# Optimization experiments

Hardware: AMD Instinct MI355X
Metric: run time of the kernel (lower is better)

The kernel has to match this reference:

```python
import jax, jax.numpy as jnp
import numpy as np

# ---- static ragged-batch / paging layout (known at trace time) ----
B = 4
Q_LENS = np.array([256, 512, 128, 384])        # new tokens per sequence
HIST = np.array([1792, 1024, 1536, 768])       # cached history per sequence
KV_LENS = Q_LENS + HIST
BS = 64                                        # paged-cache block size
NUM_BLOCKS = 128
H, D = 32, 128
HID = H * D
TOTAL_Q = int(Q_LENS.sum())                    # 1280 packed tokens
MAX_Q = int(Q_LENS.max())
MAX_KV = int(KV_LENS.max())
NBLK = (KV_LENS + BS - 1) // BS
MAX_BLOCKS = int(NBLK.max())                   # 32
ROPE_BASE = 10000.0

Q_START = np.concatenate([[0], np.cumsum(Q_LENS)[:-1]])
TOK_SEQ = np.repeat(np.arange(B), Q_LENS)                      # [TOTAL_Q]
TOK_LOCAL = np.concatenate([np.arange(l) for l in Q_LENS])     # [TOTAL_Q]
TOK_POS = (HIST[TOK_SEQ] + TOK_LOCAL).astype(np.int32)         # absolute positions

_perm = np.random.RandomState(0).permutation(NUM_BLOCKS)
BLOCK_TABLE = np.zeros((B, MAX_BLOCKS), np.int32)
_o = 0
for _i in range(B):
    BLOCK_TABLE[_i, :NBLK[_i]] = _perm[_o:_o + NBLK[_i]]
    _o += NBLK[_i]

_j = np.arange(MAX_Q)
# position of each padded query row; 0 for pad rows so the softmax row stays finite
POS_PAD = np.where(_j[None, :] < Q_LENS[:, None], HIST[:, None] + _j[None, :], 0)
KV_IDX = np.arange(MAX_KV)


def rope(x, pos):
    """HF-Llama rotary embedding on [T, heads, D] at absolute positions pos [T]."""
    half = D // 2
    inv_freq = 1.0 / (ROPE_BASE ** (jnp.arange(0, D, 2, dtype=jnp.float32) / D))
    ang = pos[:, None].astype(jnp.float32) * inv_freq[None, :]          # [T, D/2]
    cos = jnp.concatenate([jnp.cos(ang), jnp.cos(ang)], -1)[:, None, :]  # [T,1,D]
    sin = jnp.concatenate([jnp.sin(ang), jnp.sin(ang)], -1)[:, None, :]
    x1, x2 = x[..., :half], x[..., half:]
    rot = jnp.concatenate([-x2, x1], -1)                                 # rotate_half
    return x * cos + rot * sin


def setup_inputs() -> dict:
    key = jax.random.key(0)
    ks = jax.random.split(key, 7)
    s = 1.0 / np.sqrt(HID)
    return {
        'hidden_states': jax.random.normal(ks[0], (TOTAL_Q, HID), jnp.float32),
        'wq': jax.random.normal(ks[1], (HID, HID), jnp.float32) * s,
        'wk': jax.random.normal(ks[2], (HID, HID), jnp.float32) * s,
        'wv': jax.random.normal(ks[3], (HID, HID), jnp.float32) * s,
        'wo': jax.random.normal(ks[4], (HID, HID), jnp.float32) * s,
        'past_key': jax.random.normal(ks[5], (NUM_BLOCKS, BS, H, D), jnp.float32),
        'past_value': jax.random.normal(ks[6], (NUM_BLOCKS, BS, H, D), jnp.float32),
        'position_ids': jnp.asarray(TOK_POS, jnp.int32),
        'block_offsets': jnp.asarray(BLOCK_TABLE, jnp.int32),
    }


def reference(hidden_states, wq, wk, wv, wo, past_key, past_value,
              position_ids, block_offsets):
    # qkv projections (Linear without bias: x @ W.T)
    q = (hidden_states @ wq.T).reshape(TOTAL_Q, H, D)
    k = (hidden_states @ wk.T).reshape(TOTAL_Q, H, D)
    v = (hidden_states @ wv.T).reshape(TOTAL_Q, H, D)
    # inline RoPE at absolute (history + local) positions
    q = rope(q, position_ids)
    k = rope(k, position_ids)
    # fill paged KV cache via block table (context.fill_cache)
    dest = block_offsets[TOK_SEQ, position_ids // BS] * BS + position_ids % BS
    kc = past_key.reshape(NUM_BLOCKS * BS, H, D).at[dest].set(k)
    vc = past_value.reshape(NUM_BLOCKS * BS, H, D).at[dest].set(v)
    # paged gather of ragged KV per sequence: [B, MAX_KV, H, D]
    gath = block_offsets[:, KV_IDX // BS] * BS + KV_IDX[None, :] % BS
    K = kc[gath]
    V = vc[gath]
    # pad packed queries to [B, MAX_Q, H, D]
    Qp = jnp.zeros((B, MAX_Q, H, D), q.dtype).at[TOK_SEQ, TOK_LOCAL].set(q)
    scores = jnp.einsum('bqhd,bkhd->bhqk', Qp, K) / jnp.sqrt(jnp.float32(D))
    mask = KV_IDX[None, None, :] <= POS_PAD[:, :, None]   # causal + per-seq kv_len
    scores = jnp.where(mask[:, None, :, :], scores, jnp.float32(-1e30))
    attn = jax.nn.softmax(scores, axis=-1)
    out = jnp.einsum('bhqk,bkhd->bqhd', attn, V)
    # back to packed layout and output projection
    out = out[TOK_SEQ, TOK_LOCAL].reshape(TOTAL_Q, HID)
    return out @ wo.T
```

## Files before the change

### kernel.cpp

```cpp
#include <hip/hip_runtime.h>
#include <stdint.h>


typedef __attribute__((ext_vector_type(8))) short bf16x8;
typedef __attribute__((ext_vector_type(4))) float f32x4;
typedef __attribute__((ext_vector_type(4))) unsigned int u32x4;

__device__ __forceinline__ unsigned short f2bf(float f) {
  unsigned int u = __float_as_uint(f);
  u += 0x7fffu + ((u >> 16) & 1u);
  return (unsigned short)(u >> 16);
}

__global__ __launch_bounds__(256) void cvt_bf16(const float* __restrict__ src,
                                                unsigned short* __restrict__ dst, int n4) {
  int i = blockIdx.x * 256 + threadIdx.x;
  if (i >= n4) return;
  float4 v = ((const float4*)src)[i];
  ushort4 o;
  o.x = f2bf(v.x); o.y = f2bf(v.y); o.z = f2bf(v.z); o.w = f2bf(v.w);
  ((ushort4*)dst)[i] = o;
}

__device__ __forceinline__ void gload16(const void* g, void* l) {
  __builtin_amdgcn_global_load_lds(
      (const __attribute__((address_space(1))) unsigned int*)(g),
      (__attribute__((address_space(3))) unsigned int*)(l), 16, 0, 0);
}

__global__ __launch_bounds__(512, 2) void gemm256(const unsigned short* __restrict__ A,
                                                  const unsigned short* __restrict__ B,
                                                  float* __restrict__ C, int N, int K) {
  extern __shared__ char lds[];
  const int tid = threadIdx.x;
  const int lane = tid & 63;
  const int wid = tid >> 6;
  const int wm = wid >> 2, wn = wid & 3;
  const int qcol = lane & 15, g = lane >> 4;
  const int mbase = blockIdx.y * 256, nbase = blockIdx.x * 256;
  const long Kb = (long)K * 2;

  const int srow = tid >> 3;
  const int scb = ((tid & 7) * 16) ^ (((srow >> 2) & 3) << 5);
  const char* Ab = (const char*)A;
  const char* Bb = (const char*)B;
  const long asrc0 = (long)(mbase + srow) * Kb + scb;
  const long asrc1 = (long)(mbase + 64 + srow) * Kb + scb;
  const long asrc2 = (long)(mbase + 128 + srow) * Kb + scb;
  const long asrc3 = (long)(mbase + 192 + srow) * Kb + scb;
  const long bsrc0 = (long)(nbase + srow) * Kb + scb;
  const long bsrc1 = (long)(nbase + 64 + srow) * Kb + scb;
  const long bsrc2 = (long)(nbase + 128 + srow) * Kb + scb;
  const long bsrc3 = (long)(nbase + 192 + srow) * Kb + scb;
  const int dst0 = tid * 16;

#define STAGE256(kt, bs) {                                                   \
    long ko = (long)(kt) * 128;                                              \
    char* Lw = lds + (bs) * 32768;                                           \
    gload16(Ab + asrc0 + ko, Lw + dst0);                                     \
    gload16(Ab + asrc1 + ko, Lw + 8192 + dst0);                              \
    gload16(Ab + asrc2 + ko, Lw + 16384 + dst0);                             \
    gload16(Ab + asrc3 + ko, Lw + 24576 + dst0);                             \
    gload16(Bb + bsrc0 + ko, Lw + 65536 + dst0);                             \
    gload16(Bb + bsrc1 + ko, Lw + 65536 + 8192 + dst0);                      \
    gload16(Bb + bsrc2 + ko, Lw + 65536 + 16384 + dst0);                     \
    gload16(Bb + bsrc3 + ko, Lw + 65536 + 24576 + dst0);                     \
  }

  const int swl = ((qcol >> 2) & 3) << 5;
  const int c0 = (g * 16) ^ swl;
  const int c1 = (64 + g * 16) ^ swl;
  const int aoff = (wm * 128 + qcol) * 128;
  const int boff = 65536 + (wn * 64 + qcol) * 128;

  f32x4 acc[8][4];
#pragma unroll
  for (int i = 0; i < 8; ++i)
#pragma unroll
    for (int j = 0; j < 4; ++j) { acc[i][j][0]=0.f; acc[i][j][1]=0.f; acc[i][j][2]=0.f; acc[i][j][3]=0.f; }

  STAGE256(0, 0);
  const int nkt = K >> 6;
#pragma unroll 1
  for (int kt = 0; kt < nkt; ++kt) {
    const int cur = kt & 1;
    const char* Lc = lds + cur * 32768;
    if (kt + 1 < nkt) {
      STAGE256(kt + 1, cur ^ 1);
      asm volatile("s_waitcnt vmcnt(8)" ::: "memory");
    } else {
      asm volatile("s_waitcnt vmcnt(0)" ::: "memory");
    }
    __builtin_amdgcn_sched_barrier(0);
    __builtin_amdgcn_s_barrier();
    __builtin_amdgcn_sched_barrier(0);

    bf16x8 af[4][2], bfr[4][2];
#pragma unroll
    for (int mi = 0; mi < 4; ++mi) {
      af[mi][0] = *(const bf16x8*)(Lc + aoff + mi * 2048 + c0);
      af[mi][1] = *(const bf16x8*)(Lc + aoff + mi * 2048 + c1);
    }
#pragma unroll
    for (int ni = 0; ni < 2; ++ni) {
      bfr[ni][0] = *(const bf16x8*)(Lc + boff + ni * 2048 + c0);
      bfr[ni][1] = *(const bf16x8*)(Lc + boff + ni * 2048 + c1);
    }
    asm volatile("s_waitcnt lgkmcnt(0)" ::: "memory");
    __builtin_amdgcn_sched_barrier(0);
    __builtin_amdgcn_s_setprio(1);
#pragma unroll
    for (int mi = 0; mi < 4; ++mi)
#pragma unroll
      for (int ni = 0; ni < 2; ++ni) {
        acc[mi][ni] = __builtin_amdgcn_mfma_f32_16x16x32_bf16(af[mi][0], bfr[ni][0], acc[mi][ni], 0, 0, 0);
        acc[mi][ni] = __builtin_amdgcn_mfma_f32_16x16x32_bf16(af[mi][1], bfr[ni][1], acc[mi][ni], 0, 0, 0);
      }
    __builtin_amdgcn_s_setprio(0);
#pragma unroll
    for (int ni = 2; ni < 4; ++ni) {
      bfr[ni][0] = *(const bf16x8*)(Lc + boff + ni * 2048 + c0);
      bfr[ni][1] = *(const bf16x8*)(Lc + boff + ni * 2048 + c1);
    }
    asm volatile("s_waitcnt lgkmcnt(0)" ::: "memory");
    __builtin_amdgcn_sched_barrier(0);
    __builtin_amdgcn_s_setprio(1);
#pragma unroll
    for (int mi = 0; mi < 4; ++mi)
#pragma unroll
      for (int ni = 2; ni < 4; ++ni) {
        acc[mi][ni] = __builtin_amdgcn_mfma_f32_16x16x32_bf16(af[mi][0], bfr[ni][0], acc[mi][ni], 0, 0, 0);
        acc[mi][ni] = __builtin_amdgcn_mfma_f32_16x16x32_bf16(af[mi][1], bfr[ni][1], acc[mi][ni], 0, 0, 0);
      }
    __builtin_amdgcn_s_setprio(0);
#pragma unroll
    for (int mi = 0; mi < 4; ++mi) {
      af[mi][0] = *(const bf16x8*)(Lc + aoff + (mi + 4) * 2048 + c0);
      af[mi][1] = *(const bf16x8*)(Lc + aoff + (mi + 4) * 2048 + c1);
    }
    asm volatile("s_waitcnt lgkmcnt(0)" ::: "memory");
    __builtin_amdgcn_sched_barrier(0);
    __builtin_amdgcn_s_setprio(1);
#pragma unroll
    for (int mi = 0; mi < 4; ++mi)
#pragma unroll
      for (int ni = 2; ni < 4; ++ni) {
        acc[mi + 4][ni] = __builtin_amdgcn_mfma_f32_16x16x32_bf16(af[mi][0], bfr[ni][0], acc[mi + 4][ni], 0, 0, 0);
        acc[mi + 4][ni] = __builtin_amdgcn_mfma_f32_16x16x32_bf16(af[mi][1], bfr[ni][1], acc[mi + 4][ni], 0, 0, 0);
      }
    __builtin_amdgcn_s_setprio(0);
    __builtin_amdgcn_s_setprio(1);
#pragma unroll
    for (int mi = 0; mi < 4; ++mi)
#pragma unroll
      for (int ni = 0; ni < 2; ++ni) {
        acc[mi + 4][ni] = __builtin_amdgcn_mfma_f32_16x16x32_bf16(af[mi][0], bfr[ni][0], acc[mi + 4][ni], 0, 0, 0);
        acc[mi + 4][ni] = __builtin_amdgcn_mfma_f32_16x16x32_bf16(af[mi][1], bfr[ni][1], acc[mi + 4][ni], 0, 0, 0);
      }
    __builtin_amdgcn_s_setprio(0);
    __builtin_amdgcn_s_barrier();
    __builtin_amdgcn_sched_barrier(0);
  }
#undef STAGE256
  const int crow = mbase + wm * 128 + g * 4;
  const int ccol = nbase + wn * 64 + qcol;
#pragma unroll
  for (int mi = 0; mi < 8; ++mi)
#pragma unroll
    for (int ni = 0; ni < 4; ++ni)
#pragma unroll
      for (int r = 0; r < 4; ++r)
        C[(long)(crow + mi * 16 + r) * N + (ccol + ni * 16)] = acc[mi][ni][r];
}

__global__ __launch_bounds__(256, 2) void gemm_bt(const unsigned short* __restrict__ A,
                                                  const unsigned short* __restrict__ B,
                                                  float* __restrict__ C, int N, int K) {
  __shared__ unsigned short As[128 * 32] __attribute__((aligned(16)));
  __shared__ unsigned short Bs[128 * 32] __attribute__((aligned(16)));
  const int tid = threadIdx.x;
  const int lane = tid & 63;
  const int wv = tid >> 6;
  const int wr = wv >> 1, wc = wv & 1;
  const int mbase = blockIdx.y * 128, nbase = blockIdx.x * 128;
  const int r16 = lane >> 2;
  const int k8 = (lane & 3) * 8;
  const unsigned short* Ag0 = A + (mbase + wv * 32 + r16) * K + k8;
  const unsigned short* Ag1 = Ag0 + 16 * K;
  const unsigned short* Bg0 = B + (nbase + wv * 32 + r16) * K + k8;
  const unsigned short* Bg1 = Bg0 + 16 * K;
  unsigned short* Asl = As + wv * 1024 + lane * 8;
  unsigned short* Bsl = Bs + wv * 1024 + lane * 8;
  f32x4 acc[4][4];
#pragma unroll
  for (int i = 0; i < 4; ++i)
#pragma unroll
    for (int j = 0; j < 4; ++j) { acc[i][j][0]=0.f; acc[i][j][1]=0.f; acc[i][j][2]=0.f; acc[i][j][3]=0.f; }
  const int rowA = (wr * 64 + (lane & 15)) * 32 + (lane >> 4) * 8;
  const int colB = (wc * 64 + (lane & 15)) * 32 + (lane >> 4) * 8;
  for (int kt = 0; kt < K; kt += 32) {
    gload16(Ag0 + kt, Asl);
    gload16(Ag1 + kt, Asl + 512);
    gload16(Bg0 + kt, Bsl);
    gload16(Bg1 + kt, Bsl + 512);
    __syncthreads();
    bf16x8 af[4], bfr[4];
#pragma unroll
    for (int mi = 0; mi < 4; ++mi) af[mi] = *(const bf16x8*)(As + rowA + mi * 512);
#pragma unroll
    for (int ni = 0; ni < 4; ++ni) bfr[ni] = *(const bf16x8*)(Bs + colB + ni * 512);
#pragma unroll
    for (int mi = 0; mi < 4; ++mi)
#pragma unroll
      for (int ni = 0; ni < 4; ++ni)
        acc[mi][ni] = __builtin_amdgcn_mfma_f32_16x16x32_bf16(af[mi], bfr[ni], acc[mi][ni], 0, 0, 0);
    __syncthreads();
  }
  const int crow = mbase + wr * 64 + (lane >> 4) * 4;
  const int ccol = nbase + wc * 64 + (lane & 15);
#pragma unroll
  for (int mi = 0; mi < 4; ++mi)
#pragma unroll
    for (int ni = 0; ni < 4; ++ni)
#pragma unroll
      for (int r = 0; r < 4; ++r)
        C[(long)(crow + mi * 16 + r) * N + (ccol + ni * 16)] = acc[mi][ni][r];
}

__global__ __launch_bounds__(256) void rope_qk(const float* __restrict__ qkv, const int* __restrict__ pos,
                                               unsigned short* __restrict__ Qb, unsigned short* __restrict__ Kg) {
  int gw = blockIdx.x * 4 + (threadIdx.x >> 6);
  int lane = threadIdx.x & 63;
  int t = gw >> 5, h = gw & 31;
  int p = pos[t];
  int b = (t < 256) ? 0 : (t < 768) ? 1 : (t < 896) ? 2 : 3;
  float invf = exp2f(-(float)lane * 0.2076205059304601f);
  float ang = (float)p * invf;
  float sv = sinf(ang), cv = cosf(ang);
  const float* src = qkv + (long)t * 12288 + h * 128 + lane;
  float q1 = src[0], q2 = src[64];
  float k1 = src[4096], k2 = src[4096 + 64];
  const float scl = 0.08838834764831845f;
  unsigned short* qd = Qb + (long)t * 4096 + h * 128 + lane;
  qd[0]  = f2bf((q1 * cv - q2 * sv) * scl);
  qd[64] = f2bf((q2 * cv + q1 * sv) * scl);
  unsigned short* kd = Kg + ((long)(b * 32 + h) * 2048 + p) * 128 + lane;
  kd[0]  = f2bf(k1 * cv - k2 * sv);
  kd[64] = f2bf(k2 * cv + k1 * sv);
}

__global__ __launch_bounds__(256) void v_scatter(const float* __restrict__ qkv, unsigned short* __restrict__ VgT) {
  int tt = blockIdx.x, h = blockIdx.y;
  int b = (tt < 4) ? 0 : (tt < 12) ? 1 : (tt < 14) ? 2 : 3;
  int q0 = (b == 0) ? 0 : (b == 1) ? 256 : (b == 2) ? 768 : 896;
  int hist = (b == 0) ? 1792 : (b == 1) ? 1024 : (b == 2) ? 1536 : 768;
  int t0 = tt * 64;
  int jb = hist + t0 - q0;
  __shared__ unsigned short vt[64][130];
  int tid = threadIdx.x;
  int jj0 = tid >> 5, c4 = (tid & 31) * 4;
#pragma unroll
  for (int ps = 0; ps < 8; ++ps) {
    int jj = jj0 + ps * 8;
    float4 v = *(const float4*)(qkv + (long)(t0 + jj) * 12288 + 8192 + h * 128 + c4);
    ushort2 a, c;
    a.x = f2bf(v.x); a.y = f2bf(v.y); c.x = f2bf(v.z); c.y = f2bf(v.w);
    *(ushort2*)&vt[jj][c4] = a;
    *(ushort2*)&vt[jj][c4 + 2] = c;
  }
  __syncthreads();
  int d = tid >> 1, half = tid & 1;
  unsigned short* dst = VgT + ((long)(b * 32 + h) * 128 + d) * 2048 + jb + half * 32;
  int j0 = half * 32;
#pragma unroll
  for (int w = 0; w < 4; ++w) {
    uint4 u;
    u.x = vt[j0 + w * 8 + 0][d] | ((unsigned)vt[j0 + w * 8 + 1][d] << 16);
    u.y = vt[j0 + w * 8 + 2][d] | ((unsigned)vt[j0 + w * 8 + 3][d] << 16);
    u.z = vt[j0 + w * 8 + 4][d] | ((unsigned)vt[j0 + w * 8 + 5][d] << 16);
    u.w = vt[j0 + w * 8 + 6][d] | ((unsigned)vt[j0 + w * 8 + 7][d] << 16);
    ((uint4*)dst)[w] = u;
  }
}

__global__ __launch_bounds__(256) void gather_hist(const float* __restrict__ pk, const float* __restrict__ pv,
                                                   const int* __restrict__ btab,
                                                   unsigned short* __restrict__ Kg, unsigned short* __restrict__ VgT) {
  int gx = blockIdx.x, h = blockIdx.y;
  int b = (gx < 28) ? 0 : (gx < 44) ? 1 : (gx < 68) ? 2 : 3;
  int jt = gx - ((b == 0) ? 0 : (b == 1) ? 28 : (b == 2) ? 44 : 68);
  int slot0 = btab[b * 32 + jt] * 64;
  int jbase = jt * 64;
  __shared__ unsigned short vt[64][130];
  int tid = threadIdx.x;
  int jj0 = tid >> 5, c4 = (tid & 31) * 4;
#pragma unroll
  for (int ps = 0; ps < 8; ++ps) {
    int jj = jj0 + ps * 8;
    long off = ((long)(slot0 + jj) * 32 + h) * 128 + c4;
    float4 kk = *(const float4*)(pk + off);
    ushort4 ko;
    ko.x = f2bf(kk.x); ko.y = f2bf(kk.y); ko.z = f2bf(kk.z); ko.w = f2bf(kk.w);
    *(ushort4*)(Kg + ((long)(b * 32 + h) * 2048 + jbase + jj) * 128 + c4) = ko;
    float4 vv = *(const float4*)(pv + off);
    ushort2 a, c;
    a.x = f2bf(vv.x); a.y = f2bf(vv.y); c.x = f2bf(vv.z); c.y = f2bf(vv.w);
    *(ushort2*)&vt[jj][c4] = a;
    *(ushort2*)&vt[jj][c4 + 2] = c;
  }
  __syncthreads();
  int d = tid >> 1, half = tid & 1;
  unsigned short* dst = VgT + ((long)(b * 32 + h) * 128 + d) * 2048 + jbase + half * 32;
  int j0 = half * 32;
#pragma unroll
  for (int w = 0; w < 4; ++w) {
    uint4 u;
    u.x = vt[j0 + w * 8 + 0][d] | ((unsigned)vt[j0 + w * 8 + 1][d] << 16);
    u.y = vt[j0 + w * 8 + 2][d] | ((unsigned)vt[j0 + w * 8 + 3][d] << 16);
    u.z = vt[j0 + w * 8 + 4][d] | ((unsigned)vt[j0 + w * 8 + 5][d] << 16);
    u.w = vt[j0 + w * 8 + 6][d] | ((unsigned)vt[j0 + w * 8 + 7][d] << 16);
    ((uint4*)dst)[w] = u;
  }
}

__global__ __launch_bounds__(256) void attn_part(const unsigned short* __restrict__ Qb,
                                                 const unsigned short* __restrict__ Kg,
                                                 const unsigned short* __restrict__ VgT,
                                                 const int* __restrict__ pos,
                                                 float* __restrict__ Opart,
                                                 float* __restrict__ ml) {
  __shared__ char lds[32768] __attribute__((aligned(16)));
  int qt = blockIdx.x, h = blockIdx.y, ck = blockIdx.z;
  int tid = threadIdx.x;
  int wv = tid >> 6, lane = tid & 63;
  int b = (qt < 4) ? 0 : (qt < 12) ? 1 : (qt < 14) ? 2 : 3;
  int qb = qt * 64 + wv * 16;
  int qcol = lane & 15, g = lane >> 4;
  int t = qb + qcol;
  int p = pos[t];
  int pmax_wave = pos[qb + 15];
  int pmax_blk = pos[qt * 64 + 63];
  int kv_begin = ck * 512;
  if (kv_begin > pmax_blk) return;
  int kv_end = pmax_blk + 1;
  if (kv_end > kv_begin + 512) kv_end = kv_begin + 512;
  int nt = (kv_end - kv_begin + 31) >> 5;

  const char* KbhB = (const char*)(Kg + (long)(b * 32 + h) * 2048 * 128);
  const char* VbhB = (const char*)(VgT + (long)(b * 32 + h) * 128 * 2048);

  const int d0 = tid * 16, d1 = 4096 + tid * 16;
  const int ksrc0 = d0 ^ (((d0 >> 8) & 7) << 4);
  const int ksrc1 = d1 ^ (((d1 >> 8) & 7) << 4);
  const int vrow0 = d0 >> 6, vrow1 = d1 >> 6;
  const int vsrc0 = vrow0 * 4096 + ((d0 & 63) ^ ((vrow0 & 3) << 4));
  const int vsrc1 = vrow1 * 4096 + ((d1 & 63) ^ ((vrow1 & 3) << 4));

#define STAGE(kv0, buf)                                                     \
  {                                                                          \
    const char* Ksrc = KbhB + (long)(kv0) * 256;                             \
    const char* Vsrc = VbhB + (long)(kv0) * 2;                               \
    char* Kd = lds + (buf) * 8192;                                           \
    char* Vd = lds + 16384 + (buf) * 8192;                                   \
    gload16(Ksrc + ksrc0, Kd + d0);                                          \
    gload16(Ksrc + ksrc1, Kd + d1);                                          \
    gload16(Vsrc + vsrc0, Vd + d0);                                          \
    gload16(Vsrc + vsrc1, Vd + d1);                                          \
  }

  const unsigned short* Qp = Qb + (long)t * 4096 + h * 128 + g * 8;
  bf16x8 qf[4];
#pragma unroll
  for (int c = 0; c < 4; ++c) qf[c] = *(const bf16x8*)(Qp + c * 32);

  const int kswz = ((qcol & 7) << 4);
  const int vswz = (g * 16) ^ ((qcol & 3) << 4);

  float m = -1e30f, lsum = 0.f;
  f32x4 o[8];
#pragma unroll
  for (int i = 0; i < 8; ++i) { o[i][0]=0.f; o[i][1]=0.f; o[i][2]=0.f; o[i][3]=0.f; }

  STAGE(kv_begin, 0);

  for (int it = 0; it < nt; ++it) {
    int cur = it & 1;
    int kv0 = kv_begin + it * 32;
    if (it + 1 < nt) {
      STAGE(kv0 + 32, cur ^ 1);
      asm volatile("s_waitcnt vmcnt(4)" ::: "memory");
    } else {
      asm volatile("s_waitcnt vmcnt(0)" ::: "memory");
    }
    __builtin_amdgcn_sched_barrier(0);
    __builtin_amdgcn_s_barrier();
    if (kv0 <= pmax_wave) {
      const char* Kc = lds + cur * 8192;
      const char* Vc = lds + 16384 + cur * 8192;
      f32x4 s0, s1;
      s0[0]=0.f;s0[1]=0.f;s0[2]=0.f;s0[3]=0.f;
      s1[0]=0.f;s1[1]=0.f;s1[2]=0.f;s1[3]=0.f;
#pragma unroll
      for (int c = 0; c < 4; ++c) {
        int colb = (g * 16 + c * 64) ^ kswz;
        bf16x8 k0 = *(const bf16x8*)(Kc + qcol * 256 + colb);
        bf16x8 k1 = *(const bf16x8*)(Kc + 4096 + qcol * 256 + colb);
        s0 = __builtin_amdgcn_mfma_f32_16x16x32_bf16(k0, qf[c], s0, 0, 0, 0);
        s1 = __builtin_amdgcn_mfma_f32_16x16x32_bf16(k1, qf[c], s1, 0, 0, 0);
      }
      int kvg = kv0 + g * 4;
      float sv[8];
#pragma unroll
      for (int r = 0; r < 4; ++r) {
        sv[r]     = (kvg + r      <= p) ? s0[r] : -1e30f;
        sv[r + 4] = (kvg + 16 + r <= p) ? s1[r] : -1e30f;
      }
      float mt = sv[0];
#pragma unroll
      for (int i = 1; i < 8; ++i) mt = fmaxf(mt, sv[i]);
      mt = fmaxf(mt, __shfl_xor(mt, 16));
      mt = fmaxf(mt, __shfl_xor(mt, 32));
      float mnew = fmaxf(m, mt);
      float corr = __expf(m - mnew);
      float ssum = 0.f;
      float pvv[8];
#pragma unroll
      for (int i = 0; i < 8; ++i) { pvv[i] = __expf(sv[i] - mnew); ssum += pvv[i]; }
      ssum += __shfl_xor(ssum, 16);
      ssum += __shfl_xor(ssum, 32);
      lsum = lsum * corr + ssum;
      m = mnew;
#pragma unroll
      for (int df = 0; df < 8; ++df) o[df] *= corr;
      unsigned pk0 = (unsigned)f2bf(pvv[0]) | ((unsigned)f2bf(pvv[1]) << 16);
      unsigned pk1 = (unsigned)f2bf(pvv[2]) | ((unsigned)f2bf(pvv[3]) << 16);
      unsigned pk2 = (unsigned)f2bf(pvv[4]) | ((unsigned)f2bf(pvv[5]) << 16);
      unsigned pk3 = (unsigned)f2bf(pvv[6]) | ((unsigned)f2bf(pvv[7]) << 16);
      int s0l = ((g & 1) * 32) + qcol;
      int s1l = s0l + 16;
      unsigned a0 = (unsigned)__shfl((int)pk0, s0l), a1 = (unsigned)__shfl((int)pk1, s0l);
      unsigned a2 = (unsigned)__shfl((int)pk2, s0l), a3 = (unsigned)__shfl((int)pk3, s0l);
      unsigned b0 = (unsigned)__shfl((int)pk0, s1l), b1 = (unsigned)__shfl((int)pk1, s1l);
      unsigned b2 = (unsigned)__shfl((int)pk2, s1l), b3 = (unsigned)__shfl((int)pk3, s1l);
      bool hi = (g >= 2);
      u32x4 wv4;
      wv4[0] = hi ? a2 : a0; wv4[1] = hi ? a3 : a1;
      wv4[2] = hi ? b2 : b0; wv4[3] = hi ? b3 : b1;
      bf16x8 pfrag = __builtin_bit_cast(bf16x8, wv4);
#pragma unroll
      for (int df = 0; df < 8; ++df) {
        bf16x8 vf = *(const bf16x8*)(Vc + (df * 16 + qcol) * 64 + vswz);
        o[df] = __builtin_amdgcn_mfma_f32_16x16x32_bf16(vf, pfrag, o[df], 0, 0, 0);
      }
    }
    __builtin_amdgcn_s_barrier();
  }
#undef STAGE
  long pbase = (long)((qt * 32 + h) * 4 + ck);
  float* Op = Opart + pbase * 8192 + (wv * 16 + qcol) * 128 + g * 4;
#pragma unroll
  for (int df = 0; df < 8; ++df)
#pragma unroll
    for (int r = 0; r < 4; ++r)
      Op[df * 16 + r] = o[df][r];
  if (g == 0) {
    float* mlp = ml + pbase * 128 + (wv * 16 + qcol) * 2;
    mlp[0] = m;
    mlp[1] = lsum;
  }
}

__global__ __launch_bounds__(256) void attn_comb(const float* __restrict__ Opart,
                                                 const float* __restrict__ ml,
                                                 const int* __restrict__ pos,
                                                 unsigned short* __restrict__ Ao) {
  int qt = blockIdx.x, h = blockIdx.y;
  int tid = threadIdx.x;
  int q = tid >> 2, dq = (tid & 3) * 32;
  int t = qt * 64 + q;
  int p = pos[t];
  int ncv = (p >> 9) + 1;
  if (ncv > 4) ncv = 4;
  long base = (long)(qt * 32 + h) * 4;
  float M = -1e30f;
#pragma unroll
  for (int c = 0; c < 4; ++c)
    if (c < ncv) M = fmaxf(M, ml[(base + c) * 128 + q * 2]);
  float L = 0.f;
#pragma unroll
  for (int c = 0; c < 4; ++c)
    if (c < ncv) L += __expf(ml[(base + c) * 128 + q * 2] - M) * ml[(base + c) * 128 + q * 2 + 1];
  f32x4 acc[8];
#pragma unroll
  for (int i = 0; i < 8; ++i) { acc[i][0]=0.f; acc[i][1]=0.f; acc[i][2]=0.f; acc[i][3]=0.f; }
#pragma unroll
  for (int c = 0; c < 4; ++c)
    if (c < ncv) {
      float wc = __expf(ml[(base + c) * 128 + q * 2] - M);
      const f32x4* src = (const f32x4*)(Opart + (base + c) * 8192 + q * 128 + dq);
#pragma unroll
      for (int i = 0; i < 8; ++i) {
        f32x4 s = src[i];
        acc[i][0] += wc * s[0]; acc[i][1] += wc * s[1];
        acc[i][2] += wc * s[2]; acc[i][3] += wc * s[3];
      }
    }
  float inv = 1.f / L;
  unsigned short* dst = Ao + (long)t * 4096 + h * 128 + dq;
#pragma unroll
  for (int i = 0; i < 8; ++i) {
    ushort4 ov;
    ov.x = f2bf(acc[i][0] * inv); ov.y = f2bf(acc[i][1] * inv);
    ov.z = f2bf(acc[i][2] * inv); ov.w = f2bf(acc[i][3] * inv);
    *(ushort4*)(dst + i * 4) = ov;
  }
}

extern "C" void kernel_launch(void* const* d_in, const int* in_sizes, int n_in,
                              void* d_out, int out_size, void* d_ws, size_t ws_size,
                              hipStream_t stream) {
  const float* hs   = (const float*)d_in[0];
  const float* wq   = (const float*)d_in[1];
  const float* wk   = (const float*)d_in[2];
  const float* wvp  = (const float*)d_in[3];
  const float* wo   = (const float*)d_in[4];
  const float* pkey = (const float*)d_in[5];
  const float* pval = (const float*)d_in[6];
  const int* pos    = (const int*)d_in[7];
  const int* btab   = (const int*)d_in[8];

  unsigned short* Wqkv = (unsigned short*)d_ws;
  unsigned short* Wo   = Wqkv + (size_t)12288 * 4096;
  unsigned short* Hb   = Wo + (size_t)4096 * 4096;
  float* qkv           = (float*)(Hb + (size_t)1280 * 4096);
  unsigned short* Qbf  = (unsigned short*)(qkv + (size_t)1280 * 12288);
  unsigned short* Kg   = Qbf + (size_t)1280 * 4096;
  unsigned short* VgT  = Kg + (size_t)4 * 32 * 2048 * 128;
  unsigned short* Aob  = VgT + (size_t)4 * 32 * 2048 * 128;
  float* Opart = (float*)d_ws;
  float* mlb   = (float*)((char*)d_ws + 83886080);
  if (ws_size < 362807296ull) return;

  cvt_bf16<<<16384, 256, 0, stream>>>(wq,  Wqkv,                 4194304);
  cvt_bf16<<<16384, 256, 0, stream>>>(wk,  Wqkv + 16777216,      4194304);
  cvt_bf16<<<16384, 256, 0, stream>>>(wvp, Wqkv + 33554432,      4194304);
  cvt_bf16<<<16384, 256, 0, stream>>>(wo,  Wo,                   4194304);
  cvt_bf16<<<5120,  256, 0, stream>>>(hs,  Hb,                   1310720);

  gemm256<<<dim3(48, 5), 512, 131072, stream>>>(Hb, Wqkv, qkv, 12288, 4096);
  rope_qk<<<10240, 256, 0, stream>>>(qkv, pos, Qbf, Kg);
  v_scatter<<<dim3(20, 32), 256, 0, stream>>>(qkv, VgT);
  gather_hist<<<dim3(80, 32), 256, 0, stream>>>(pkey, pval, btab, Kg, VgT);
  attn_part<<<dim3(20, 32, 4), 256, 0, stream>>>(Qbf, Kg, VgT, pos, Opart, mlb);
  attn_comb<<<dim3(20, 32), 256, 0, stream>>>(Opart, mlb, pos, Aob);
  gemm_bt<<<dim3(32, 10), 256, 0, stream>>>(Aob, Wo, (float*)d_out, 4096, 4096);
}
```

Measured before the change: 495.4 us.

## Restructure gemm256 into half-tile staged ping-pong pipeline with XOR swizzle

Measured after the change: 472.7 us. 4.6% less time.

```diff
diff --git a/kernel.cpp b/kernel.cpp
--- a/kernel.cpp
+++ b/kernel.cpp
@@ -27,6 +27,8 @@
       (const __attribute__((address_space(1))) unsigned int*)(g),
       (__attribute__((address_space(3))) unsigned int*)(l), 16, 0, 0);
 }
+
+#define MFMA_BF16(a, b, c) __builtin_amdgcn_mfma_f32_16x16x32_bf16((a), (b), (c), 0, 0, 0)
 
 __global__ __launch_bounds__(512, 2) void gemm256(const unsigned short* __restrict__ A,
                                                   const unsigned short* __restrict__ B,
@@ -39,39 +41,25 @@
   const int qcol = lane & 15, g = lane >> 4;
   const int mbase = blockIdx.y * 256, nbase = blockIdx.x * 256;
   const long Kb = (long)K * 2;
-
-  const int srow = tid >> 3;
-  const int scb = ((tid & 7) * 16) ^ (((srow >> 2) & 3) << 5);
+  const int ktmax = (K >> 6) - 1;
+
   const char* Ab = (const char*)A;
   const char* Bb = (const char*)B;
-  const long asrc0 = (long)(mbase + srow) * Kb + scb;
-  const long asrc1 = (long)(mbase + 64 + srow) * Kb + scb;
-  const long asrc2 = (long)(mbase + 128 + srow) * Kb + scb;
-  const long asrc3 = (long)(mbase + 192 + srow) * Kb + scb;
-  const long bsrc0 = (long)(nbase + srow) * Kb + scb;
-  const long bsrc1 = (long)(nbase + 64 + srow) * Kb + scb;
-  const long bsrc2 = (long)(nbase + 128 + srow) * Kb + scb;
-  const long bsrc3 = (long)(nbase + 192 + srow) * Kb + scb;
-  const int dst0 = tid * 16;
-
-#define STAGE256(kt, bs) {                                                   \
-    long ko = (long)(kt) * 128;                                              \
-    char* Lw = lds + (bs) * 32768;                                           \
-    gload16(Ab + asrc0 + ko, Lw + dst0);                                     \
-    gload16(Ab + asrc1 + ko, Lw + 8192 + dst0);                              \
-    gload16(Ab + asrc2 + ko, Lw + 16384 + dst0);                             \
-    gload16(Ab + asrc3 + ko, Lw + 24576 + dst0);                             \
-    gload16(Bb + bsrc0 + ko, Lw + 65536 + dst0);                             \
-    gload16(Bb + bsrc1 + ko, Lw + 65536 + 8192 + dst0);                      \
-    gload16(Bb + bsrc2 + ko, Lw + 65536 + 16384 + dst0);                     \
-    gload16(Bb + bsrc3 + ko, Lw + 65536 + 24576 + dst0);                     \
-  }
-
-  const int swl = ((qcol >> 2) & 3) << 5;
-  const int c0 = (g * 16) ^ swl;
-  const int c1 = (64 + g * 16) ^ swl;
-  const int aoff = (wm * 128 + qcol) * 128;
-  const int boff = 65536 + (wn * 64 + qcol) * 128;
+  const int srow = tid >> 3;
+  const int ssw = ((tid & 7) ^ (srow & 7)) * 16;
+
+#define STG_HT(MB, GB, HF, BUF, KT) {                                          \
+    long ro = (long)((GB) + (HF) * 128 + srow) * Kb + (long)(KT) * 128 + ssw;  \
+    char* d = lds + (BUF) * 65536 + (MB) * 32768 + (HF) * 16384 + tid * 16;    \
+    const char* sp = (MB) ? Bb : Ab;                                           \
+    gload16(sp + ro, d);                                                       \
+    gload16(sp + ro + 64 * Kb, d + 8192);                                      \
+  }
+
+  const int aoffB = wm * 16384 + qcol * 128;
+  const int boffB = 32768 + (wn >> 1) * 16384 + ((wn & 1) * 64 + qcol) * 128;
+  const int swk0 = ((g) ^ (qcol & 7)) * 16;
+  const int swk1 = ((4 + g) ^ (qcol & 7)) * 16;
 
   f32x4 acc[8][4];
 #pragma unroll
@@ -79,89 +67,176 @@
 #pragma unroll
     for (int j = 0; j < 4; ++j) { acc[i][j][0]=0.f; acc[i][j][1]=0.f; acc[i][j][2]=0.f; acc[i][j][3]=0.f; }
 
-  STAGE256(0, 0);
-  const int nkt = K >> 6;
+#define BARRIER() { __builtin_amdgcn_sched_barrier(0); __builtin_amdgcn_s_barrier(); }
+#define LGKM0()   { asm volatile("s_waitcnt lgkmcnt(0)" ::: "memory"); __builtin_amdgcn_sched_barrier(0); }
+#define VM4()     { asm volatile("s_waitcnt vmcnt(4)" ::: "memory"); __builtin_amdgcn_sched_barrier(0); }
+
+  STG_HT(0, mbase, 0, 0, 0); STG_HT(0, mbase, 1, 0, 0);
+  STG_HT(1, nbase, 0, 0, 0); STG_HT(1, nbase, 1, 0, 0);
+  STG_HT(1, nbase, 0, 1, 1); STG_HT(1, nbase, 1, 1, 1);
+  VM4();
+  __builtin_amdgcn_s_barrier();
+
+  const int nit = K >> 7;
 #pragma unroll 1
-  for (int kt = 0; kt < nkt; ++kt) {
-    const int cur = kt & 1;
-    const char* Lc = lds + cur * 32768;
-    if (kt + 1 < nkt) {
-      STAGE256(kt + 1, cur ^ 1);
-      asm volatile("s_waitcnt vmcnt(8)" ::: "memory");
-    } else {
-      asm volatile("s_waitcnt vmcnt(0)" ::: "memory");
-    }
-    __builtin_amdgcn_sched_barrier(0);
-    __builtin_amdgcn_s_barrier();
-    __builtin_amdgcn_sched_barrier(0);
-
-    bf16x8 af[4][2], bfr[4][2];
+  for (int t = 0; t < nit; ++t) {
+    const int e = 2 * t, o = 2 * t + 1;
+    const int e2 = (e + 2 > ktmax) ? ktmax : e + 2;
+    const int o2 = (o + 2 > ktmax) ? ktmax : o + 2;
+    const char* L0 = lds;
+    const char* L1 = lds + 65536;
+    bf16x8 af[4][2], bfv[4][2];
+
 #pragma unroll
     for (int mi = 0; mi < 4; ++mi) {
-      af[mi][0] = *(const bf16x8*)(Lc + aoff + mi * 2048 + c0);
-      af[mi][1] = *(const bf16x8*)(Lc + aoff + mi * 2048 + c1);
+      af[mi][0] = *(const bf16x8*)(L0 + aoffB + mi * 2048 + swk0);
+      af[mi][1] = *(const bf16x8*)(L0 + aoffB + mi * 2048 + swk1);
     }
 #pragma unroll
     for (int ni = 0; ni < 2; ++ni) {
-      bfr[ni][0] = *(const bf16x8*)(Lc + boff + ni * 2048 + c0);
-      bfr[ni][1] = *(const bf16x8*)(Lc + boff + ni * 2048 + c1);
-    }
-    asm volatile("s_waitcnt lgkmcnt(0)" ::: "memory");
-    __builtin_amdgcn_sched_barrier(0);
+      bfv[ni][0] = *(const bf16x8*)(L0 + boffB + ni * 2048 + swk0);
+      bfv[ni][1] = *(const bf16x8*)(L0 + boffB + ni * 2048 + swk1);
+    }
+    STG_HT(0, mbase, 0, 1, o);
+    BARRIER(); LGKM0();
     __builtin_amdgcn_s_setprio(1);
 #pragma unroll
     for (int mi = 0; mi < 4; ++mi)
 #pragma unroll
       for (int ni = 0; ni < 2; ++ni) {
-        acc[mi][ni] = __builtin_amdgcn_mfma_f32_16x16x32_bf16(af[mi][0], bfr[ni][0], acc[mi][ni], 0, 0, 0);
-        acc[mi][ni] = __builtin_amdgcn_mfma_f32_16x16x32_bf16(af[mi][1], bfr[ni][1], acc[mi][ni], 0, 0, 0);
-      }
-    __builtin_amdgcn_s_setprio(0);
+        acc[mi][ni] = MFMA_BF16(af[mi][0], bfv[ni][0], acc[mi][ni]);
+        acc[mi][ni] = MFMA_BF16(af[mi][1], bfv[ni][1], acc[mi][ni]);
+      }
+    __builtin_amdgcn_s_setprio(0);
+    BARRIER();
+
 #pragma unroll
     for (int ni = 2; ni < 4; ++ni) {
-      bfr[ni][0] = *(const bf16x8*)(Lc + boff + ni * 2048 + c0);
-      bfr[ni][1] = *(const bf16x8*)(Lc + boff + ni * 2048 + c1);
-    }
-    asm volatile("s_waitcnt lgkmcnt(0)" ::: "memory");
-    __builtin_amdgcn_sched_barrier(0);
+      bfv[ni][0] = *(const bf16x8*)(L0 + boffB + ni * 2048 + swk0);
+      bfv[ni][1] = *(const bf16x8*)(L0 + boffB + ni * 2048 + swk1);
+    }
+    STG_HT(0, mbase, 1, 1, o);
+    BARRIER(); LGKM0();
     __builtin_amdgcn_s_setprio(1);
 #pragma unroll
     for (int mi = 0; mi < 4; ++mi)
 #pragma unroll
       for (int ni = 2; ni < 4; ++ni) {
-        acc[mi][ni] = __builtin_amdgcn_mfma_f32_16x16x32_bf16(af[mi][0], bfr[ni][0], acc[mi][ni], 0, 0, 0);
-        acc[mi][ni] = __builtin_amdgcn_mfma_f32_16x16x32_bf16(af[mi][1], bfr[ni][1], acc[mi][ni], 0, 0, 0);
-      }
-    __builtin_amdgcn_s_setprio(0);
+        acc[mi][ni] = MFMA_BF16(af[mi][0], bfv[ni][0], acc[mi][ni]);
+        acc[mi][ni] = MFMA_BF16(af[mi][1], bfv[ni][1], acc[mi][ni]);
+      }
+    __builtin_amdgcn_s_setprio(0);
+    BARRIER();
+
 #pragma unroll
     for (int mi = 0; mi < 4; ++mi) {
-      af[mi][0] = *(const bf16x8*)(Lc + aoff + (mi + 4) * 2048 + c0);
-      af[mi][1] = *(const bf16x8*)(Lc + aoff + (mi + 4) * 2048 + c1);
-    }
-    asm volatile("s_waitcnt lgkmcnt(0)" ::: "memory");
-    __builtin_amdgcn_sched_barrier(0);
+      af[mi][0] = *(const bf16x8*)(L0 + aoffB + (mi + 4) * 2048 + swk0);
+      af[mi][1] = *(const bf16x8*)(L0 + aoffB + (mi + 4) * 2048 + swk1);
+    }
+    STG_HT(1, nbase, 0, 0, e2);
+    BARRIER(); LGKM0();
     __builtin_amdgcn_s_setprio(1);
 #pragma unroll
     for (int mi = 0; mi < 4; ++mi)
 #pragma unroll
       for (int ni = 2; ni < 4; ++ni) {
-        acc[mi + 4][ni] = __builtin_amdgcn_mfma_f32_16x16x32_bf16(af[mi][0], bfr[ni][0], acc[mi + 4][ni], 0, 0, 0);
-        acc[mi + 4][ni] = __builtin_amdgcn_mfma_f32_16x16x32_bf16(af[mi][1], bfr[ni][1], acc[mi + 4][ni], 0, 0, 0);
-      }
-    __builtin_amdgcn_s_setprio(0);
+        acc[mi + 4][ni] = MFMA_BF16(af[mi][0], bfv[ni][0], acc[mi + 4][ni]);
+        acc[mi + 4][ni] = MFMA_BF16(af[mi][1], bfv[ni][1], acc[mi + 4][ni]);
+      }
+    __builtin_amdgcn_s_setprio(0);
+    BARRIER();
+
+    STG_HT(1, nbase, 1, 0, e2);
+    VM4();
+    BARRIER();
     __builtin_amdgcn_s_setprio(1);
 #pragma unroll
     for (int mi = 0; mi < 4; ++mi)
 #pragma unroll
       for (int ni = 0; ni < 2; ++ni) {
-        acc[mi + 4][ni] = __builtin_amdgcn_mfma_f32_16x16x32_bf16(af[mi][0], bfr[ni][0], acc[mi + 4][ni], 0, 0, 0);
-        acc[mi + 4][ni] = __builtin_amdgcn_mfma_f32_16x16x32_bf16(af[mi][1], bfr[ni][1], acc[mi + 4][ni], 0, 0, 0);
-      }
-    __builtin_amdgcn_s_setprio(0);
-    __builtin_amdgcn_s_barrier();
-    __builtin_amdgcn_sched_barrier(0);
-  }
-#undef STAGE256
+        acc[mi + 4][ni] = MFMA_BF16(af[mi][0], bfv[ni][0], acc[mi + 4][ni]);
+        acc[mi + 4][ni] = MFMA_BF16(af[mi][1], bfv[ni][1], acc[mi + 4][ni]);
+      }
+    __builtin_amdgcn_s_setprio(0);
+    BARRIER();
+
+#pragma unroll
+    for (int mi = 0; mi < 4; ++mi) {
+      af[mi][0] = *(const bf16x8*)(L1 + aoffB + mi * 2048 + swk0);
+      af[mi][1] = *(const bf16x8*)(L1 + aoffB + mi * 2048 + swk1);
+    }
+#pragma unroll
+    for (int ni = 0; ni < 2; ++ni) {
+      bfv[ni][0] = *(const bf16x8*)(L1 + boffB + ni * 2048 + swk0);
+      bfv[ni][1] = *(const bf16x8*)(L1 + boffB + ni * 2048 + swk1);
+    }
+    STG_HT(0, mbase, 0, 0, e2);
+    BARRIER(); LGKM0();
+    __builtin_amdgcn_s_setprio(1);
+#pragma unroll
+    for (int mi = 0; mi < 4; ++mi)
+#pragma unroll
+      for (int ni = 0; ni < 2; ++ni) {
+        acc[mi][ni] = MFMA_BF16(af[mi][0], bfv[ni][0], acc[mi][ni]);
+        acc[mi][ni] = MFMA_BF16(af[mi][1], bfv[ni][1], acc[mi][ni]);
+      }
+    __builtin_amdgcn_s_setprio(0);
+    BARRIER();
+
+#pragma unroll
+    for (int ni = 2; ni < 4; ++ni) {
+      bfv[ni][0] = *(const bf16x8*)(L1 + boffB + ni * 2048 + swk0);
+      bfv[ni][1] = *(const bf16x8*)(L1 + boffB + ni * 2048 + swk1);
+    }
+    STG_HT(0, mbase, 1, 0, e2);
+    BARRIER(); LGKM0();
+    __builtin_amdgcn_s_setprio(1);
+#pragma unroll
+    for (int mi = 0; mi < 4; ++mi)
+#pragma unroll
+      for (int ni = 2; ni < 4; ++ni) {
+        acc[mi][ni] = MFMA_BF16(af[mi][0], bfv[ni][0], acc[mi][ni]);
+        acc[mi][ni] = MFMA_BF16(af[mi][1], bfv[ni][1], acc[mi][ni]);
+      }
+    __builtin_amdgcn_s_setprio(0);
+    BARRIER();
+
+#pragma unroll
+    for (int mi = 0; mi < 4; ++mi) {
+      af[mi][0] = *(const bf16x8*)(L1 + aoffB + (mi + 4) * 2048 + swk0);
+      af[mi][1] = *(const bf16x8*)(L1 + aoffB + (mi + 4) * 2048 + swk1);
+    }
+    STG_HT(1, nbase, 0, 1, o2);
+    BARRIER(); LGKM0();
+    __builtin_amdgcn_s_setprio(1);
+#pragma unroll
+    for (int mi = 0; mi < 4; ++mi)
+#pragma unroll
+      for (int ni = 2; ni < 4; ++ni) {
+        acc[mi + 4][ni] = MFMA_BF16(af[mi][0], bfv[ni][0], acc[mi + 4][ni]);
+        acc[mi + 4][ni] = MFMA_BF16(af[mi][1], bfv[ni][1], acc[mi + 4][ni]);
+      }
+    __builtin_amdgcn_s_setprio(0);
+    BARRIER();
+
+    STG_HT(1, nbase, 1, 1, o2);
+    VM4();
+    BARRIER();
+    __builtin_amdgcn_s_setprio(1);
+#pragma unroll
+    for (int mi = 0; mi < 4; ++mi)
+#pragma unroll
+      for (int ni = 0; ni < 2; ++ni) {
+        acc[mi + 4][ni] = MFMA_BF16(af[mi][0], bfv[ni][0], acc[mi + 4][ni]);
+        acc[mi + 4][ni] = MFMA_BF16(af[mi][1], bfv[ni][1], acc[mi + 4][ni]);
+      }
+    __builtin_amdgcn_s_setprio(0);
+    BARRIER();
+  }
+#undef STG_HT
+#undef BARRIER
+#undef LGKM0
+#undef VM4
   const int crow = mbase + wm * 128 + g * 4;
   const int ccol = nbase + wn * 64 + qcol;
 #pragma unroll
@@ -213,7 +288,7 @@
     for (int mi = 0; mi < 4; ++mi)
 #pragma unroll
       for (int ni = 0; ni < 4; ++ni)
-        acc[mi][ni] = __builtin_amdgcn_mfma_f32_16x16x32_bf16(af[mi], bfr[ni], acc[mi][ni], 0, 0, 0);
+        acc[mi][ni] = MFMA_BF16(af[mi], bfr[ni], acc[mi][ni]);
     __syncthreads();
   }
   const int crow = mbase + wr * 64 + (lane >> 4) * 4;
@@ -405,8 +480,8 @@
         int colb = (g * 16 + c * 64) ^ kswz;
         bf16x8 k0 = *(const bf16x8*)(Kc + qcol * 256 + colb);
         bf16x8 k1 = *(const bf16x8*)(Kc + 4096 + qcol * 256 + colb);
-        s0 = __builtin_amdgcn_mfma_f32_16x16x32_bf16(k0, qf[c], s0, 0, 0, 0);
-        s1 = __builtin_amdgcn_mfma_f32_16x16x32_bf16(k1, qf[c], s1, 0, 0, 0);
+        s0 = MFMA_BF16(k0, qf[c], s0);
+        s1 = MFMA_BF16(k1, qf[c], s1);
       }
       int kvg = kv0 + g * 4;
       float sv[8];
@@ -450,7 +525,7 @@
 #pragma unroll
       for (int df = 0; df < 8; ++df) {
         bf16x8 vf = *(const bf16x8*)(Vc + (df * 16 + qcol) * 64 + vswz);
-        o[df] = __builtin_amdgcn_mfma_f32_16x16x32_bf16(vf, pfrag, o[df], 0, 0, 0);
+        o[df] = MFMA_BF16(vf, pfrag, o[df]);
       }
     }
     __builtin_amdgcn_s_barrier();
```
